# Performance work log

Hardware: AMD Instinct MI355X
Metric: run time of the kernel (lower is better)

The kernel has to match this reference:

```python
import jax, jax.numpy as jnp
import numpy as np

H, HD, RD = 16, 128, 64          # n_heads, head_dim, rope_dim
CD = HD - RD                      # content_dim = 64
THETA = 10000.0


def apply_rope(x, cos, sin):
    # x: [B,H,T,RD]; cos/sin: [T,RD//2] broadcast over B,H
    d = x.shape[-1] // 2
    x1, x2 = x[..., :d], x[..., d:]
    return jnp.concatenate([x1 * cos - x2 * sin, x1 * sin + x2 * cos], axis=-1)


def setup_inputs() -> dict:
    key = jax.random.key(0)
    ks = jax.random.split(key, 9)
    d_model, q_rank, d_latent = 2048, 512, 512
    B, T = 2, 2048
    s = 0.02
    return {
        "x": jax.random.normal(ks[0], (B, T, d_model), dtype=jnp.float32),
        "Wq_down": jax.random.normal(ks[1], (d_model, q_rank), dtype=jnp.float32) * s,
        "Wq_up": jax.random.normal(ks[2], (q_rank, H * CD), dtype=jnp.float32) * s,
        "Wq_rope": jax.random.normal(ks[3], (d_model, H * RD), dtype=jnp.float32) * s,
        "Wkv_down": jax.random.normal(ks[4], (d_model, d_latent), dtype=jnp.float32) * s,
        "Wk_up": jax.random.normal(ks[5], (d_latent, H * CD), dtype=jnp.float32) * s,
        "Wv_up": jax.random.normal(ks[6], (d_latent, H * HD), dtype=jnp.float32) * s,
        "Wk_rope": jax.random.normal(ks[7], (d_model, H * RD), dtype=jnp.float32) * s,
        "Wo": jax.random.normal(ks[8], (H * HD, d_model), dtype=jnp.float32) * s,
    }


def reference(x, Wq_down, Wq_up, Wq_rope, Wkv_down, Wk_up, Wv_up, Wk_rope, Wo):
    B, T, _ = x.shape

    # low-rank projections
    q_content = (x @ Wq_down) @ Wq_up            # [B,T,H*CD]
    q_pos = x @ Wq_rope                          # [B,T,H*RD]
    kv_latent = x @ Wkv_down                     # [B,T,d_latent]
    k_content = kv_latent @ Wk_up                # [B,T,H*CD]
    k_pos = x @ Wk_rope                          # [B,T,H*RD]
    v = kv_latent @ Wv_up                        # [B,T,H*HD]

    def split_heads(t, d):
        return t.reshape(B, T, H, d).transpose(0, 2, 1, 3)  # [B,H,T,d]

    q_content = split_heads(q_content, CD)
    q_pos = split_heads(q_pos, RD)
    k_content = split_heads(k_content, CD)
    k_pos = split_heads(k_pos, RD)
    v = split_heads(v, HD)

    # rotary tables: [T, RD//2]
    inv_freq = 1.0 / (THETA ** (jnp.arange(0, RD, 2, dtype=jnp.float32) / RD))
    freqs = jnp.arange(T, dtype=jnp.float32)[:, None] * inv_freq[None, :]
    cos, sin = jnp.cos(freqs), jnp.sin(freqs)

    q_pos = apply_rope(q_pos, cos, sin)
    k_pos = apply_rope(k_pos, cos, sin)

    q = jnp.concatenate([q_content, q_pos], axis=-1)  # [B,H,T,HD]
    k = jnp.concatenate([k_content, k_pos], axis=-1)  # [B,H,T,HD]

    # causal SDPA, scale = 1/sqrt(head_dim)
    scale = 1.0 / jnp.sqrt(jnp.asarray(HD, dtype=q.dtype))
    scores = jnp.einsum("bhqd,bhkd->bhqk", q, k) * scale
    causal = jnp.tril(jnp.ones((T, T), dtype=bool))
    scores = jnp.where(causal, scores, jnp.finfo(scores.dtype).min)
    attn = jax.nn.softmax(scores, axis=-1)
    out = jnp.einsum("bhqk,bhkd->bhqd", attn, v)      # [B,H,T,HD]

    out = out.transpose(0, 2, 1, 3).reshape(B, T, H * HD)
    return out @ Wo
```

## Files before the change

### kernel.cpp

```cpp
#include <hip/hip_runtime.h>
#include <hip/hip_bf16.h>
#include <stdint.h>
#include <math.h>

#define H_ 16
#define HD_ 128
#define RD_ 64
#define CD_ 64
#define DM_ 2048
#define QR_ 512
#define DL_ 512
#define B_ 2
#define T_ 2048
#define M_TOT (B_*T_)

typedef __attribute__((ext_vector_type(8))) short short8;
typedef __attribute__((ext_vector_type(4))) float f32x4;
typedef __attribute__((ext_vector_type(16))) float f32x16;

__device__ __forceinline__ unsigned short f2b_hw(float f){
  __hip_bfloat16 h = __float2bfloat16(f);
  union { __hip_bfloat16 h; unsigned short u; } c; c.h = h; return c.u;
}
__device__ __forceinline__ float b2f(unsigned short b){
  union { unsigned u; float f; } a; a.u = ((unsigned)b) << 16;
  return a.f;
}
__device__ __forceinline__ unsigned pack2(float lo, float hi){
  __hip_bfloat162 h2 = __float22bfloat162_rn(make_float2(lo, hi));
  union { __hip_bfloat162 h; unsigned u; } c; c.h = h2; return c.u;
}

#define GLOAD16(g, l) __builtin_amdgcn_global_load_lds( \
    (__attribute__((address_space(1))) void*)(g), \
    (__attribute__((address_space(3))) void*)(l), 16, 0, 0)

__global__ void cast_f32_bf16(const float* __restrict__ src,
                              unsigned short* __restrict__ dst, int n){
  int i = (blockIdx.x * blockDim.x + threadIdx.x) * 4;
  if (i < n){
    float4 v = *(const float4*)(src + i);
    ushort4 o;
    o.x = f2b_hw(v.x); o.y = f2b_hw(v.y); o.z = f2b_hw(v.z); o.w = f2b_hw(v.w);
    *(ushort4*)(dst + i) = o;
  }
}

__global__ void rope_table(float2* __restrict__ tab){
  int idx = blockIdx.x * 256 + threadIdx.x;
  int t = idx >> 5, j = idx & 31;
  float invf = exp2f(-(float)j * 0.4152410118750f);
  float fr = (float)t * invf;
  float s, c;
  sincosf(fr, &s, &c);
  tab[idx] = make_float2(c, s);
}

struct TTe { const float* src; unsigned short* dst; int K, N, blk0; };
struct TT8 { TTe e[8]; };

__global__ void transpose_cast8(TT8 tab){
  __shared__ float tile[32][33];
  int bid = blockIdx.x;
  const float* src = tab.e[0].src;
  unsigned short* dst = tab.e[0].dst;
  int K = tab.e[0].K, N = tab.e[0].N, loc = bid;
  #pragma unroll
  for (int j = 1; j < 8; j++){
    if (bid >= tab.e[j].blk0){
      src = tab.e[j].src; dst = tab.e[j].dst;
      K = tab.e[j].K; N = tab.e[j].N; loc = bid - tab.e[j].blk0;
    }
  }
  int cols = N / 32;
  int n0 = (loc % cols) * 32, k0 = (loc / cols) * 32;
  int tx = threadIdx.x, ty = threadIdx.y;
  #pragma unroll
  for (int r = ty; r < 32; r += 8)
    tile[r][tx] = src[(size_t)(k0 + r) * N + n0 + tx];
  __syncthreads();
  #pragma unroll
  for (int r = ty; r < 32; r += 8)
    dst[(size_t)(n0 + r) * K + k0 + tx] = f2b_hw(tile[tx][r]);
}

template<int MODE>
__global__ __launch_bounds__(256) void gemm_bt(
    const unsigned short* __restrict__ A, int lda,
    const unsigned short* __restrict__ Bt,
    void* __restrict__ Cv, void* __restrict__ Cv2, void* __restrict__ Cv3,
    const float2* __restrict__ tab,
    int ldc, int N, int K)
{
  __shared__ unsigned short As[128 * 32];
  __shared__ unsigned short Bs[128 * 32];
  int tid = threadIdx.x;

  int gx = gridDim.x;
  int nwg = gx * gridDim.y;
  int lin = blockIdx.x + gx * blockIdx.y;
  int q8 = nwg >> 3;
  int nl = (lin & 7) * q8 + (lin >> 3);
  int m0 = (nl / gx) * 128, n0 = (nl % gx) * 128;

  int lane = tid & 63, w = tid >> 6;
  int wr = (w >> 1) * 64, wc = (w & 1) * 64;
  int mr = lane & 15, kg = lane >> 4;

  const unsigned short* Aeff = A;
  if (MODE == 5 && n0 >= 1024) Aeff = A + 512;

  const unsigned short* Ag = Aeff + (size_t)(m0 + (tid >> 2)) * lda + ((tid & 3) << 3);
  const unsigned short* Bg = Bt   + (size_t)(n0 + (tid >> 2)) * K + ((tid & 3) << 3);

  f32x4 acc[4][4];
  #pragma unroll
  for (int i = 0; i < 4; i++)
    #pragma unroll
    for (int j = 0; j < 4; j++)
      acc[i][j] = (f32x4){0.f, 0.f, 0.f, 0.f};

  for (int k0 = 0; k0 < K; k0 += 32) {
    #pragma unroll
    for (int j = 0; j < 2; j++) {
      GLOAD16(Ag + (size_t)j * 64 * lda, &As[j * 2048 + tid * 8]);
      GLOAD16(Bg + (size_t)j * 64 * K, &Bs[j * 2048 + tid * 8]);
    }
    Ag += 32; Bg += 32;
    __syncthreads();
    short8 af[4], bf[4];
    #pragma unroll
    for (int i = 0; i < 4; i++)
      af[i] = *(const short8*)&As[(wr + i * 16 + mr) * 32 + kg * 8];
    #pragma unroll
    for (int j = 0; j < 4; j++)
      bf[j] = *(const short8*)&Bs[(wc + j * 16 + mr) * 32 + kg * 8];
    __builtin_amdgcn_s_setprio(1);
    #pragma unroll
    for (int i = 0; i < 4; i++)
      #pragma unroll
      for (int j = 0; j < 4; j++)
        acc[i][j] = __builtin_amdgcn_mfma_f32_16x16x32_bf16(af[i], bf[j], acc[i][j], 0, 0, 0);
    __builtin_amdgcn_s_setprio(0);
    __syncthreads();
  }

  if (MODE == 1) {
    float* C = (float*)Cv;
    #pragma unroll
    for (int i = 0; i < 4; i++)
      #pragma unroll
      for (int j = 0; j < 4; j++)
        #pragma unroll
        for (int r = 0; r < 4; r++) {
          int row = m0 + wr + i * 16 + kg * 4 + r;
          int col = n0 + wc + j * 16 + mr;
          C[(size_t)row * ldc + col] = acc[i][j][r];
        }
  } else if (MODE == 4) {
    if (n0 < 1024) {
      unsigned short* C = (unsigned short*)Cv;
      #pragma unroll
      for (int i = 0; i < 4; i++)
        #pragma unroll
        for (int j = 0; j < 4; j++)
          #pragma unroll
          for (int r = 0; r < 4; r++) {
            int row = m0 + wr + i * 16 + kg * 4 + r;
            int col = n0 + wc + j * 16 + mr;
            C[(size_t)row * ldc + col] = f2b_hw(acc[i][j][r]);
          }
    } else {
      const bool isq = (n0 < 2048);
      unsigned short* dst = (unsigned short*)(isq ? Cv2 : Cv3);
      int cbase = n0 - (isq ? 1024 : 2048);
      #pragma unroll
      for (int jp = 0; jp < 2; jp++) {
        int colA = wc + jp * 16 + mr;
        int cA = cbase + colA;
        int h = cA >> 6, jr = cA & 63;
        #pragma unroll
        for (int i = 0; i < 4; i++)
          #pragma unroll
          for (int r = 0; r < 4; r++) {
            int gr = m0 + wr + i * 16 + kg * 4 + r;
            int t = gr & (T_ - 1);
            float2 cs = tab[t * 32 + jr];
            float x1 = acc[i][jp][r], x2 = acc[i][jp + 2][r];
            size_t base = ((size_t)((gr >> 11) * H_ + h) * T_ + t) * 128 + 64;
            dst[base + jr]      = f2b_hw(x1 * cs.x - x2 * cs.y);
            dst[base + jr + 32] = f2b_hw(x1 * cs.y + x2 * cs.x);
          }
      }
    }
  } else {
    if (n0 < 2048) {
      unsigned short* dstp = (unsigned short*)(n0 < 1024 ? Cv : Cv2);
      int cb = (n0 < 1024) ? n0 : n0 - 1024;
      #pragma unroll
      for (int i = 0; i < 4; i++)
        #pragma unroll
        for (int j = 0; j < 4; j++) {
          int colb = cb + wc + j * 16 + mr;
          int h = colb >> 6, d = colb & 63;
          #pragma unroll
          for (int r = 0; r < 4; r++) {
            int gr = m0 + wr + i * 16 + kg * 4 + r;
            size_t idx = ((size_t)((gr >> 11) * H_ + h) * T_ + (gr & (T_-1))) * 128 + d;
            dstp[idx] = f2b_hw(acc[i][j][r]);
          }
        }
    } else {
      unsigned short* vtp = (unsigned short*)Cv3;
      #pragma unroll
      for (int i = 0; i < 4; i++)
        #pragma unroll
        for (int j = 0; j < 4; j++) {
          int c2 = n0 + wc + j * 16 + mr - 2048;
          int h = c2 >> 7, d = c2 & 127;
          int gr0 = m0 + wr + i * 16 + kg * 4;
          int b = gr0 >> 11, t0 = gr0 & (T_-1);
          ushort4 o;
          o.x = f2b_hw(acc[i][j][0]); o.y = f2b_hw(acc[i][j][1]);
          o.z = f2b_hw(acc[i][j][2]); o.w = f2b_hw(acc[i][j][3]);
          size_t idx = ((size_t)(b * H_ + h) * 128 + d) * T_ + t0;
          *(ushort4*)&vtp[idx] = o;
        }
    }
  }
}

__global__ __launch_bounds__(256, 2) void attn_fwd7(
    const unsigned short* __restrict__ qh,
    const unsigned short* __restrict__ kh,
    const unsigned short* __restrict__ vt,
    unsigned short* __restrict__ ao)
{
  __shared__ __align__(16) unsigned short lds[4 * 8192];

  const int tid  = threadIdx.x;
  const int lane = tid & 63, w = tid >> 6;
  const int l31  = lane & 31, hi = lane >> 5;
  const int bh = blockIdx.y;
  const int b  = bh >> 4, hd = bh & 15;
  int qt = blockIdx.x;
  if (bh >= 16) qt = 15 - qt;
  const int q0w   = qt * 128 + w * 32;
  const int qg    = q0w + l31;
  const int qmaxw = q0w + 31;
  const int nt    = 2 * qt + 2;

  const unsigned short* Qg = qh + (size_t)bh * T_ * 128;
  const unsigned short* Kg = kh + (size_t)bh * T_ * 128;
  const unsigned short* Vg = vt + (size_t)bh * 128 * T_;

  short8 qf[8];
  #pragma unroll
  for (int kc = 0; kc < 8; kc++)
    qf[kc] = *(const short8*)&Qg[(size_t)qg * 128 + kc * 16 + hi * 8];

  f32x16 accO[4];
  #pragma unroll
  for (int sb = 0; sb < 4; sb++)
    #pragma unroll
    for (int r = 0; r < 16; r++) accO[sb][r] = 0.f;

  float m = -1e30f, lsum = 0.f;
  const float SC = 0.12751743f;

  int krow[4], kwof[4], vrow[4], vwof[4];
  #pragma unroll
  for (int jj = 0; jj < 4; jj++){
    int r_ = (w * 4 + jj) * 4 + (lane >> 4);
    krow[jj] = r_;
    kwof[jj] = r_ * 128 + ((((lane & 15) * 16) ^ ((r_ & 7) << 4)) >> 1);
    int d_ = (w * 4 + jj) * 8 + (lane >> 3);
    vrow[jj] = d_;
    vwof[jj] = d_ * 64 + ((((lane & 7) * 16) ^ ((d_ & 7) << 4)) >> 1);
  }
  const int kcol = (lane & 15) * 8;
  const int vcol = (lane & 7) * 8;

  uint4 kst[4], vst[4];

#define REG_LOAD(kvt) do {                                                    \
    int kv0s = (kvt) * 64;                                                    \
    _Pragma("unroll")                                                         \
    for (int j_ = 0; j_ < 4; j_++) {                                          \
      kst[j_] = *(const uint4*)&Kg[(size_t)(kv0s + krow[j_]) * 128 + kcol];   \
      vst[j_] = *(const uint4*)&Vg[(size_t)vrow[j_] * T_ + kv0s + vcol];      \
    }                                                                         \
  } while (0)

#define DS_WRITE(bufi) do {                                                   \
    unsigned short* ksb_ = lds + (bufi) * 8192;                               \
    unsigned short* vsb_ = lds + 16384 + (bufi) * 8192;                       \
    _Pragma("unroll")                                                         \
    for (int j_ = 0; j_ < 4; j_++) {                                          \
      *(uint4*)&ksb_[kwof[j_]] = kst[j_];                                     \
      *(uint4*)&vsb_[vwof[j_]] = vst[j_];                                     \
    }                                                                         \
  } while (0)

  REG_LOAD(0);
  DS_WRITE(0);
  if (nt > 1) REG_LOAD(1);
  asm volatile("s_waitcnt lgkmcnt(0)" ::: "memory");
  __builtin_amdgcn_s_barrier();
  __builtin_amdgcn_sched_barrier(0);

  for (int t = 0; t < nt; t++) {
    const int cur = t & 1;
    if (t + 1 < nt) DS_WRITE(cur ^ 1);
    if (t + 2 < nt) REG_LOAD(t + 2);
    const int kv0 = t * 64;
    if (kv0 <= qmaxw) {
      const unsigned short* Kb = lds + cur * 8192;
      const unsigned short* Vb = lds + 16384 + cur * 8192;

      f32x16 sa0, sa1;
      #pragma unroll
      for (int r = 0; r < 16; r++) { sa0[r] = 0.f; sa1[r] = 0.f; }
      __builtin_amdgcn_s_setprio(1);
      #pragma unroll
      for (int kc = 0; kc < 8; kc++) {
        int co = (kc * 32 + hi * 16);
        int r0 = l31;
        short8 kf0 = *(const short8*)&Kb[r0 * 128 + ((co ^ ((r0 & 7) << 4)) >> 1)];
        sa0 = __builtin_amdgcn_mfma_f32_32x32x16_bf16(kf0, qf[kc], sa0, 0, 0, 0);
        int r1 = 32 + l31;
        short8 kf1 = *(const short8*)&Kb[r1 * 128 + ((co ^ ((r1 & 7) << 4)) >> 1)];
        sa1 = __builtin_amdgcn_mfma_f32_32x32x16_bf16(kf1, qf[kc], sa1, 0, 0, 0);
      }
      __builtin_amdgcn_s_setprio(0);

      float p0[16], p1[16];
      float pmax = -1e30f;
      bool needMask = (kv0 + 63 > q0w);
      if (needMask) {
        #pragma unroll
        for (int r = 0; r < 16; r++) {
          int crow = (r & 3) + 8 * (r >> 2) + 4 * hi;
          float v0 = sa0[r] * SC;
          float v1 = sa1[r] * SC;
          if (kv0 + crow > qg)      v0 = -1e30f;
          if (kv0 + 32 + crow > qg) v1 = -1e30f;
          p0[r] = v0; p1[r] = v1;
          pmax = fmaxf(pmax, fmaxf(v0, v1));
        }
      } else {
        #pragma unroll
        for (int r = 0; r < 16; r++) {
          float v0 = sa0[r] * SC;
          float v1 = sa1[r] * SC;
          p0[r] = v0; p1[r] = v1;
          pmax = fmaxf(pmax, fmaxf(v0, v1));
        }
      }
      pmax = fmaxf(pmax, __shfl_xor(pmax, 32, 64));
      if (!__all(pmax <= m + 8.f)) {
        float mn  = fmaxf(m, pmax);
        float fac = exp2f(m - mn);
        m = mn;
        lsum *= fac;
        #pragma unroll
        for (int sb = 0; sb < 4; sb++)
          #pragma unroll
          for (int r = 0; r < 16; r++) accO[sb][r] *= fac;
      }
      float ls = 0.f;
      #pragma unroll
      for (int r = 0; r < 16; r++) {
        p0[r] = exp2f(p0[r] - m);
        p1[r] = exp2f(p1[r] - m);
        ls += p0[r] + p1[r];
      }
      ls += __shfl_xor(ls, 32, 64);
      lsum += ls;

      #pragma unroll
      for (int kc2 = 0; kc2 < 4; kc2++) {
        unsigned A01, A23, B01, B23;
        if (kc2 == 0) { A01 = pack2(p0[0], p0[1]);  A23 = pack2(p0[2], p0[3]);
                        B01 = pack2(p0[4], p0[5]);  B23 = pack2(p0[6], p0[7]); }
        else if (kc2 == 1) { A01 = pack2(p0[8], p0[9]);   A23 = pack2(p0[10], p0[11]);
                             B01 = pack2(p0[12], p0[13]); B23 = pack2(p0[14], p0[15]); }
        else if (kc2 == 2) { A01 = pack2(p1[0], p1[1]);  A23 = pack2(p1[2], p1[3]);
                             B01 = pack2(p1[4], p1[5]);  B23 = pack2(p1[6], p1[7]); }
        else { A01 = pack2(p1[8], p1[9]);   A23 = pack2(p1[10], p1[11]);
               B01 = pack2(p1[12], p1[13]); B23 = pack2(p1[14], p1[15]); }
        asm("v_permlane32_swap_b32 %0, %1" : "+v"(A01), "+v"(B01));
        asm("v_permlane32_swap_b32 %0, %1" : "+v"(A23), "+v"(B23));
        union { unsigned u[4]; short8 v; } pk;
        pk.u[0] = A01; pk.u[1] = A23; pk.u[2] = B01; pk.u[3] = B23;
        short8 pa = pk.v;
        __builtin_amdgcn_s_setprio(1);
        #pragma unroll
        for (int sb = 0; sb < 4; sb++) {
          int d = sb * 32 + l31;
          short8 vf = *(const short8*)&Vb[d * 64 + (((kc2 * 32 + hi * 16) ^ ((d & 7) << 4)) >> 1)];
          accO[sb] = __builtin_amdgcn_mfma_f32_32x32x16_bf16(vf, pa, accO[sb], 0, 0, 0);
        }
        __builtin_amdgcn_s_setprio(0);
      }
    }
    __builtin_amdgcn_sched_barrier(0);
    asm volatile("s_waitcnt lgkmcnt(0)" ::: "memory");
    __builtin_amdgcn_s_barrier();
    __builtin_amdgcn_sched_barrier(0);
  }

  float rl = 1.0f / lsum;
  size_t orow = ((size_t)b * T_ + qg) * (H_*HD_) + hd * 128;
  #pragma unroll
  for (int sb = 0; sb < 4; sb++)
    #pragma unroll
    for (int g = 0; g < 4; g++) {
      ushort4 o;
      o.x = f2b_hw(accO[sb][4 * g + 0] * rl);
      o.y = f2b_hw(accO[sb][4 * g + 1] * rl);
      o.z = f2b_hw(accO[sb][4 * g + 2] * rl);
      o.w = f2b_hw(accO[sb][4 * g + 3] * rl);
      *(ushort4*)&ao[orow + sb * 32 + 8 * g + 4 * hi] = o;
    }
#undef REG_LOAD
#undef DS_WRITE
}

extern "C" void kernel_launch(void* const* d_in, const int* in_sizes, int n_in,
                              void* d_out, int out_size, void* d_ws, size_t ws_size,
                              hipStream_t stream)
{
  (void)in_sizes; (void)n_in; (void)out_size; (void)ws_size;
  const float* x        = (const float*)d_in[0];
  const float* Wq_down  = (const float*)d_in[1];
  const float* Wq_up    = (const float*)d_in[2];
  const float* Wq_rope  = (const float*)d_in[3];
  const float* Wkv_down = (const float*)d_in[4];
  const float* Wk_up    = (const float*)d_in[5];
  const float* Wv_up    = (const float*)d_in[6];
  const float* Wk_rope  = (const float*)d_in[7];
  const float* Wo       = (const float*)d_in[8];

  char* ws = (char*)d_ws;
  unsigned short* xb      = (unsigned short*)(ws + 0);
  unsigned short* Wdall   = (unsigned short*)(ws + 16777216);
  unsigned short* WquT    = (unsigned short*)(ws + 29360128);
  unsigned short* WkcvT   = (unsigned short*)(ws + 30408704);
  unsigned short* WoT     = (unsigned short*)(ws + 33554432);
  unsigned short* projall = (unsigned short*)(ws + 41943040);
  unsigned short* qh      = (unsigned short*)(ws + 67108864);
  unsigned short* kh      = (unsigned short*)(ws + 83886080);
  unsigned short* vt      = (unsigned short*)(ws + 100663296);
  unsigned short* ao      = (unsigned short*)(ws + 117440512);
  float2*         ctab    = (float2*)(ws + 134217728);

  dim3 tb(32, 8);

  cast_f32_bf16<<<(M_TOT * DM_ / 4 + 255) / 256, 256, 0, stream>>>(x, xb, M_TOT * DM_);
  rope_table<<<256, 256, 0, stream>>>(ctab);

  TT8 tab;
  int blk = 0;
  tab.e[0] = { Wq_down,  Wdall,               DM_, QR_,     blk }; blk += (QR_/32)*(DM_/32);
  tab.e[1] = { Wkv_down, Wdall + 512*2048,    DM_, DL_,     blk }; blk += (DL_/32)*(DM_/32);
  tab.e[2] = { Wq_rope,  Wdall + 1024*2048,   DM_, H_*RD_,  blk }; blk += (H_*RD_/32)*(DM_/32);
  tab.e[3] = { Wk_rope,  Wdall + 2048*2048,   DM_, H_*RD_,  blk }; blk += (H_*RD_/32)*(DM_/32);
  tab.e[4] = { Wq_up,    WquT,                QR_, H_*CD_,  blk }; blk += (H_*CD_/32)*(QR_/32);
  tab.e[5] = { Wk_up,    WkcvT,               DL_, H_*CD_,  blk }; blk += (H_*CD_/32)*(DL_/32);
  tab.e[6] = { Wv_up,    WkcvT + 1024*512,    DL_, H_*HD_,  blk }; blk += (H_*HD_/32)*(DL_/32);
  tab.e[7] = { Wo,       WoT,                 H_*HD_, DM_,  blk }; blk += (DM_/32)*(H_*HD_/32);
  transpose_cast8<<<blk, tb, 0, stream>>>(tab);

  gemm_bt<4><<<dim3(3072/128, M_TOT/128), 256, 0, stream>>>(
      xb, DM_, Wdall, projall, qh, kh, ctab, 1024, 3072, DM_);
  gemm_bt<5><<<dim3(4096/128, M_TOT/128), 256, 0, stream>>>(
      projall, 1024, WquT, qh, kh, vt, nullptr, 0, 4096, DL_);

  attn_fwd7<<<dim3(16, 32), 256, 0, stream>>>(qh, kh, vt, ao);

  gemm_bt<1><<<dim3(DM_/128, M_TOT/128), 256, 0, stream>>>(
      ao, 2048, WoT, d_out, nullptr, nullptr, nullptr, DM_, DM_, H_*HD_);
}
```

Measured before the change: 345.1 us.

## Add 256x256-tile double-buffered GEMM with swizzled LDS for projection kernels

Adds a new gemm256 kernel that uses 512 threads, 256x256 output tiles, a K-step of 64, double-buffered LDS staging with explicit vmcnt waits, and XOR-swizzled LDS addressing. The two projection GEMMs (down-projection with rope epilogue, and up-projection writing head layouts) now use it, while the output projection keeps the old 128-tile kernel. The aim is more data reuse per tile and loads overlapped with MFMA work. In exchange it uses 128KB of LDS at one block per CU and launches far fewer blocks (192 and 256), which may leave CUs idle.

Measured after the change: 312.0 us. 1.11x faster.

```diff
diff --git a/kernel.cpp b/kernel.cpp
--- a/kernel.cpp
+++ b/kernel.cpp
@@ -88,9 +88,7 @@
 __global__ __launch_bounds__(256) void gemm_bt(
     const unsigned short* __restrict__ A, int lda,
     const unsigned short* __restrict__ Bt,
-    void* __restrict__ Cv, void* __restrict__ Cv2, void* __restrict__ Cv3,
-    const float2* __restrict__ tab,
-    int ldc, int N, int K)
+    void* __restrict__ Cv, int ldc, int N, int K)
 {
   __shared__ unsigned short As[128 * 32];
   __shared__ unsigned short Bs[128 * 32];
@@ -107,11 +105,8 @@
   int wr = (w >> 1) * 64, wc = (w & 1) * 64;
   int mr = lane & 15, kg = lane >> 4;
 
-  const unsigned short* Aeff = A;
-  if (MODE == 5 && n0 >= 1024) Aeff = A + 512;
-
-  const unsigned short* Ag = Aeff + (size_t)(m0 + (tid >> 2)) * lda + ((tid & 3) << 3);
-  const unsigned short* Bg = Bt   + (size_t)(n0 + (tid >> 2)) * K + ((tid & 3) << 3);
+  const unsigned short* Ag = A  + (size_t)(m0 + (tid >> 2)) * lda + ((tid & 3) << 3);
+  const unsigned short* Bg = Bt + (size_t)(n0 + (tid >> 2)) * K + ((tid & 3) << 3);
 
   f32x4 acc[4][4];
   #pragma unroll
@@ -157,37 +152,142 @@
           int col = n0 + wc + j * 16 + mr;
           C[(size_t)row * ldc + col] = acc[i][j][r];
         }
-  } else if (MODE == 4) {
+  }
+}
+
+template<int MODE>
+__global__ __launch_bounds__(512, 1) void gemm256(
+    const unsigned short* __restrict__ A, int lda,
+    const unsigned short* __restrict__ Bt,
+    void* __restrict__ Cv, void* __restrict__ Cv2, void* __restrict__ Cv3,
+    const float2* __restrict__ tab,
+    int ldc, int N, int K)
+{
+  __shared__ __align__(16) unsigned short lds[65536];
+  char* ldsb = (char*)lds;
+
+  const int tid = threadIdx.x;
+  const int lane = tid & 63, w = tid >> 6;
+  const int wm = w >> 2, wn = w & 3;
+  const int l15 = lane & 15, kg = lane >> 4;
+
+  int gx = gridDim.x;
+  int nwg = gx * gridDim.y;
+  int lin = blockIdx.x + gx * blockIdx.y;
+  int q8 = nwg >> 3;
+  int nl = (lin & 7) * q8 + (lin >> 3);
+  int m0 = (nl / gx) * 256, n0 = (nl % gx) * 256;
+
+  const unsigned short* Aeff = A;
+  if (MODE == 5 && n0 >= 1024) Aeff = A + 512;
+
+  const int srow = tid >> 3;
+  const int scol = ((((tid & 7) << 4) ^ (((tid >> 5) & 1) << 5)) >> 1);
+  const int aswz = ((l15 >> 2) & 1) << 5;
+
+#define STG(bufb, kt) do {                                                     \
+    int k0_ = (kt) * 64;                                                       \
+    _Pragma("unroll")                                                          \
+    for (int h_ = 0; h_ < 2; h_++)                                             \
+      _Pragma("unroll")                                                        \
+      for (int i_ = 0; i_ < 2; i_++) {                                         \
+        GLOAD16(Aeff + (size_t)(m0 + h_*128 + i_*64 + srow) * lda + k0_ + scol,\
+                ldsb + (bufb)*65536 + h_*16384 + i_*8192 + tid*16);            \
+        GLOAD16(Bt + (size_t)(n0 + h_*128 + i_*64 + srow) * K + k0_ + scol,    \
+                ldsb + (bufb)*65536 + 32768 + h_*16384 + i_*8192 + tid*16);    \
+      }                                                                        \
+  } while (0)
+
+  f32x4 acc[8][4];
+  #pragma unroll
+  for (int i = 0; i < 8; i++)
+    #pragma unroll
+    for (int j = 0; j < 4; j++)
+      acc[i][j] = (f32x4){0.f, 0.f, 0.f, 0.f};
+
+  const int nK = K >> 6;
+  STG(0, 0);
+  STG(1, 1);
+
+  for (int t = 0; t < nK; t++) {
+    const int c = t & 1;
+    if (t < nK - 1) { asm volatile("s_waitcnt vmcnt(8)" ::: "memory"); }
+    else            { asm volatile("s_waitcnt vmcnt(0)" ::: "memory"); }
+    __builtin_amdgcn_s_barrier();
+    __builtin_amdgcn_sched_barrier(0);
+
+    const char* bufA = ldsb + c * 65536 + wm * 16384;
+    const char* bufB = ldsb + c * 65536 + 32768;
+
+    short8 bfr[4][2];
+    #pragma unroll
+    for (int nf = 0; nf < 4; nf++) {
+      int nr = wn * 64 + nf * 16 + l15;
+      #pragma unroll
+      for (int kk = 0; kk < 2; kk++) {
+        int L = (nr & 127) * 128 + kk * 64 + kg * 16;
+        bfr[nf][kk] = *(const short8*)(bufB + (nr >> 7) * 16384 + (L ^ aswz));
+      }
+    }
+    __builtin_amdgcn_s_setprio(1);
+    #pragma unroll
+    for (int mh = 0; mh < 2; mh++) {
+      short8 afr[4][2];
+      #pragma unroll
+      for (int q = 0; q < 4; q++) {
+        int mf = mh * 4 + q;
+        #pragma unroll
+        for (int kk = 0; kk < 2; kk++) {
+          int L = (mf * 16 + l15) * 128 + kk * 64 + kg * 16;
+          afr[q][kk] = *(const short8*)(bufA + (L ^ aswz));
+        }
+      }
+      #pragma unroll
+      for (int q = 0; q < 4; q++)
+        #pragma unroll
+        for (int nf = 0; nf < 4; nf++)
+          #pragma unroll
+          for (int kk = 0; kk < 2; kk++)
+            acc[mh*4+q][nf] = __builtin_amdgcn_mfma_f32_16x16x32_bf16(
+                afr[q][kk], bfr[nf][kk], acc[mh*4+q][nf], 0, 0, 0);
+    }
+    __builtin_amdgcn_s_setprio(0);
+    __builtin_amdgcn_sched_barrier(0);
+    __builtin_amdgcn_s_barrier();
+    __builtin_amdgcn_sched_barrier(0);
+    if (t + 2 < nK) STG(c, t + 2);
+  }
+#undef STG
+
+  if (MODE == 4) {
     if (n0 < 1024) {
       unsigned short* C = (unsigned short*)Cv;
       #pragma unroll
-      for (int i = 0; i < 4; i++)
-        #pragma unroll
-        for (int j = 0; j < 4; j++)
+      for (int mf = 0; mf < 8; mf++)
+        #pragma unroll
+        for (int nf = 0; nf < 4; nf++)
           #pragma unroll
-          for (int r = 0; r < 4; r++) {
-            int row = m0 + wr + i * 16 + kg * 4 + r;
-            int col = n0 + wc + j * 16 + mr;
-            C[(size_t)row * ldc + col] = f2b_hw(acc[i][j][r]);
+          for (int rr = 0; rr < 4; rr++) {
+            int row = m0 + wm * 128 + mf * 16 + kg * 4 + rr;
+            int col = n0 + wn * 64 + nf * 16 + l15;
+            C[(size_t)row * ldc + col] = f2b_hw(acc[mf][nf][rr]);
           }
     } else {
       const bool isq = (n0 < 2048);
       unsigned short* dst = (unsigned short*)(isq ? Cv2 : Cv3);
-      int cbase = n0 - (isq ? 1024 : 2048);
-      #pragma unroll
-      for (int jp = 0; jp < 2; jp++) {
-        int colA = wc + jp * 16 + mr;
-        int cA = cbase + colA;
-        int h = cA >> 6, jr = cA & 63;
-        #pragma unroll
-        for (int i = 0; i < 4; i++)
+      int hbase = ((n0 - (isq ? 1024 : 2048)) >> 6) + wn;
+      #pragma unroll
+      for (int nf = 0; nf < 2; nf++) {
+        int jr = nf * 16 + l15;
+        #pragma unroll
+        for (int mf = 0; mf < 8; mf++)
           #pragma unroll
-          for (int r = 0; r < 4; r++) {
-            int gr = m0 + wr + i * 16 + kg * 4 + r;
-            int t = gr & (T_ - 1);
-            float2 cs = tab[t * 32 + jr];
-            float x1 = acc[i][jp][r], x2 = acc[i][jp + 2][r];
-            size_t base = ((size_t)((gr >> 11) * H_ + h) * T_ + t) * 128 + 64;
+          for (int rr = 0; rr < 4; rr++) {
+            int gr = m0 + wm * 128 + mf * 16 + kg * 4 + rr;
+            int tt = gr & (T_ - 1), bb = gr >> 11;
+            float2 cs = tab[tt * 32 + jr];
+            float x1 = acc[mf][nf][rr], x2 = acc[mf][nf + 2][rr];
+            size_t base = ((size_t)(bb * H_ + hbase) * T_ + tt) * 128 + 64;
             dst[base + jr]      = f2b_hw(x1 * cs.x - x2 * cs.y);
             dst[base + jr + 32] = f2b_hw(x1 * cs.y + x2 * cs.x);
           }
@@ -196,36 +296,36 @@
   } else {
     if (n0 < 2048) {
       unsigned short* dstp = (unsigned short*)(n0 < 1024 ? Cv : Cv2);
-      int cb = (n0 < 1024) ? n0 : n0 - 1024;
-      #pragma unroll
-      for (int i = 0; i < 4; i++)
-        #pragma unroll
-        for (int j = 0; j < 4; j++) {
-          int colb = cb + wc + j * 16 + mr;
-          int h = colb >> 6, d = colb & 63;
+      int cb0 = n0 - (n0 < 1024 ? 0 : 1024);
+      #pragma unroll
+      for (int nf = 0; nf < 4; nf++) {
+        int colb = cb0 + wn * 64 + nf * 16 + l15;
+        int h = colb >> 6, d = colb & 63;
+        #pragma unroll
+        for (int mf = 0; mf < 8; mf++)
           #pragma unroll
-          for (int r = 0; r < 4; r++) {
-            int gr = m0 + wr + i * 16 + kg * 4 + r;
+          for (int rr = 0; rr < 4; rr++) {
+            int gr = m0 + wm * 128 + mf * 16 + kg * 4 + rr;
             size_t idx = ((size_t)((gr >> 11) * H_ + h) * T_ + (gr & (T_-1))) * 128 + d;
-            dstp[idx] = f2b_hw(acc[i][j][r]);
+            dstp[idx] = f2b_hw(acc[mf][nf][rr]);
           }
-        }
+      }
     } else {
       unsigned short* vtp = (unsigned short*)Cv3;
       #pragma unroll
-      for (int i = 0; i < 4; i++)
-        #pragma unroll
-        for (int j = 0; j < 4; j++) {
-          int c2 = n0 + wc + j * 16 + mr - 2048;
-          int h = c2 >> 7, d = c2 & 127;
-          int gr0 = m0 + wr + i * 16 + kg * 4;
-          int b = gr0 >> 11, t0 = gr0 & (T_-1);
+      for (int nf = 0; nf < 4; nf++) {
+        int c2 = n0 + wn * 64 + nf * 16 + l15 - 2048;
+        int h = c2 >> 7, d = c2 & 127;
+        #pragma unroll
+        for (int mf = 0; mf < 8; mf++) {
+          int gr0 = m0 + wm * 128 + mf * 16 + kg * 4;
+          int bb = gr0 >> 11, t0 = gr0 & (T_-1);
           ushort4 o;
-          o.x = f2b_hw(acc[i][j][0]); o.y = f2b_hw(acc[i][j][1]);
-          o.z = f2b_hw(acc[i][j][2]); o.w = f2b_hw(acc[i][j][3]);
-          size_t idx = ((size_t)(b * H_ + h) * 128 + d) * T_ + t0;
-          *(ushort4*)&vtp[idx] = o;
+          o.x = f2b_hw(acc[mf][nf][0]); o.y = f2b_hw(acc[mf][nf][1]);
+          o.z = f2b_hw(acc[mf][nf][2]); o.w = f2b_hw(acc[mf][nf][3]);
+          *(ushort4*)&vtp[((size_t)(bb * H_ + h) * 128 + d) * T_ + t0] = o;
         }
+      }
     }
   }
 }
@@ -472,13 +572,13 @@
   tab.e[7] = { Wo,       WoT,                 H_*HD_, DM_,  blk }; blk += (DM_/32)*(H_*HD_/32);
   transpose_cast8<<<blk, tb, 0, stream>>>(tab);
 
-  gemm_bt<4><<<dim3(3072/128, M_TOT/128), 256, 0, stream>>>(
+  gemm256<4><<<dim3(3072/256, M_TOT/256), 512, 0, stream>>>(
       xb, DM_, Wdall, projall, qh, kh, ctab, 1024, 3072, DM_);
-  gemm_bt<5><<<dim3(4096/128, M_TOT/128), 256, 0, stream>>>(
+  gemm256<5><<<dim3(4096/256, M_TOT/256), 512, 0, stream>>>(
       projall, 1024, WquT, qh, kh, vt, nullptr, 0, 4096, DL_);
 
   attn_fwd7<<<dim3(16, 32), 256, 0, stream>>>(qh, kh, vt, ao);
 
   gemm_bt<1><<<dim3(DM_/128, M_TOT/128), 256, 0, stream>>>(
-      ao, 2048, WoT, d_out, nullptr, nullptr, nullptr, DM_, DM_, H_*HD_);
-}
+      ao, 2048, WoT, d_out, DM_, DM_, H_*HD_);
+}
```
